# Optimization experiments

Hardware: AMD Instinct MI355X
Metric: run time of the kernel (lower is better)

Reference implementation:

```python
import jax, jax.numpy as jnp
import numpy as np

ALPHA = 0.1
K = 10


def setup_inputs() -> dict:
    key = jax.random.key(0)
    ks = jax.random.split(key, 8)
    N, E, F_IN, H, C = 100000, 1600000, 256, 128, 16
    features = jax.random.normal(ks[0], (N, F_IN), dtype=jnp.float32)
    # Kaiming-ish small init so activations stay sane
    W0 = jax.random.normal(ks[1], (F_IN, H), dtype=jnp.float32) * (1.0 / np.sqrt(F_IN))
    b0 = jnp.zeros((H,), jnp.float32)
    W1 = jax.random.normal(ks[2], (H, H), dtype=jnp.float32) * (1.0 / np.sqrt(H))
    b1 = jnp.zeros((H,), jnp.float32)
    W2 = jax.random.normal(ks[3], (H, C), dtype=jnp.float32) * (1.0 / np.sqrt(H))
    b2 = jnp.zeros((C,), jnp.float32)
    src = jax.random.randint(ks[4], (E,), 0, N, dtype=jnp.int32)
    dst = jax.random.randint(ks[5], (E,), 0, N, dtype=jnp.int32)
    return {"features": features, "W0": W0, "b0": b0, "W1": W1, "b1": b1,
            "W2": W2, "b2": b2, "src": src, "dst": dst}


def reference(features, W0, b0, W1, b1, W2, b2, src, dst):
    N = features.shape[0]
    # --- MLP feature transform (feat_drop=0 -> identity) ---
    h = jax.nn.relu(features @ W0 + b0)
    h = jax.nn.relu(h @ W1 + b1)
    h = h @ W2 + b2  # [N, C]
    # --- symmetric normalization D_out^{-1/2} A D_in^{-1/2} (DGL APPNPConv) ---
    ones = jnp.ones(src.shape[0], dtype=h.dtype)
    out_deg = jax.ops.segment_sum(ones, src, num_segments=N)
    in_deg = jax.ops.segment_sum(ones, dst, num_segments=N)
    norm_src = jnp.where(out_deg > 0, jax.lax.rsqrt(jnp.maximum(out_deg, 1.0)), 0.0)[:, None]
    norm_dst = jnp.where(in_deg > 0, jax.lax.rsqrt(jnp.maximum(in_deg, 1.0)), 0.0)[:, None]
    # --- K-step personalized PageRank propagation (edge_drop=0) ---
    h0 = h
    for _ in range(K):
        msg = (h * norm_src)[src]                         # gather [E, C]
        agg = jax.ops.segment_sum(msg, dst, num_segments=N)  # scatter-add [N, C]
        h = (1.0 - ALPHA) * (agg * norm_dst) + ALPHA * h0
    return h
```

## Files before the change

### kernel.cpp

```cpp
#include <hip/hip_runtime.h>

typedef _Float16 half8 __attribute__((ext_vector_type(8)));
typedef _Float16 half4 __attribute__((ext_vector_type(4)));
typedef float f32x4 __attribute__((ext_vector_type(4)));
typedef unsigned short u16;
typedef unsigned int u32;

constexpr int F_IN = 256;
constexpr int H    = 128;
constexpr int C    = 16;
constexpr int KITER = 10;

constexpr int RANGE = 16384;
constexpr int PCH   = 128;


__global__ __launch_bounds__(256) void hist_k(const int* __restrict__ idx,
                                              u16* __restrict__ partial,
                                              int N, int E, int R, int chunk) {
    __shared__ unsigned int cnt[RANGE / 2];
    const int p  = blockIdx.x / R;
    const int r  = blockIdx.x % R;
    const int lo = r * RANGE;
    const int hi = min(lo + RANGE, N);
    const int t  = threadIdx.x;
    for (int i = t; i < RANGE / 2; i += 256) cnt[i] = 0;
    __syncthreads();
    const int e0 = p * chunk, e1 = min(e0 + chunk, E);
    for (int e = e0 + t; e < e1; e += 256) {
        int d = idx[e];
        if (d >= lo && d < hi) {
            int dl = d - lo;
            atomicAdd(&cnt[dl >> 1], 1u << ((dl & 1) << 4));
        }
    }
    __syncthreads();
    for (int i = lo + t; i < hi; i += 256) {
        int il = i - lo;
        partial[(size_t)p * N + i] = (u16)(cnt[il >> 1] >> ((il & 1) << 4));
    }
}

__global__ __launch_bounds__(256) void hist_rank_k(const int* __restrict__ idx,
                                                   u16* __restrict__ partial,
                                                   u16* __restrict__ rank16,
                                                   int N, int E, int R, int chunk) {
    __shared__ unsigned int cnt[RANGE / 2];
    const int p  = blockIdx.x / R;
    const int r  = blockIdx.x % R;
    const int lo = r * RANGE;
    const int hi = min(lo + RANGE, N);
    const int t  = threadIdx.x;
    for (int i = t; i < RANGE / 2; i += 256) cnt[i] = 0;
    __syncthreads();
    const int e0 = p * chunk, e1 = min(e0 + chunk, E);
    for (int e = e0 + t; e < e1; e += 256) {
        int d = idx[e];
        if (d >= lo && d < hi) {
            int dl    = d - lo;
            int shift = (dl & 1) << 4;
            unsigned int old = atomicAdd(&cnt[dl >> 1], 1u << shift);
            rank16[e] = (u16)((old >> shift) & 0xffffu);
        }
    }
    __syncthreads();
    for (int i = lo + t; i < hi; i += 256) {
        int il = i - lo;
        partial[(size_t)p * N + i] = (u16)(cnt[il >> 1] >> ((il & 1) << 4));
    }
}

__global__ __launch_bounds__(256) void colsum_k(const u16* __restrict__ partial,
                                                int* __restrict__ deg, int N) {
    int i = blockIdx.x * 256 + threadIdx.x;
    if (i < N) {
        int s = 0;
#pragma unroll 8
        for (int p = 0; p < PCH; ++p) s += partial[(size_t)p * N + i];
        deg[i] = s;
    }
}

__global__ __launch_bounds__(256) void colprefix_norm_k(u16* __restrict__ partial,
                                                        const int* __restrict__ dego,
                                                        int* __restrict__ degi,
                                                        float* __restrict__ ns,
                                                        float* __restrict__ nd, int N) {
    int i = blockIdx.x * 256 + threadIdx.x;
    if (i < N) {
        int run = 0;
        for (int p = 0; p < PCH; ++p) {
            size_t q = (size_t)p * N + i;
            int v = partial[q];
            partial[q] = (u16)run;
            run += v;
        }
        degi[i] = run;
        int a = dego[i];
        ns[i] = (a > 0) ? rsqrtf((float)a) : 0.0f;
        nd[i] = (run > 0) ? rsqrtf((float)run) : 0.0f;
    }
}


__global__ __launch_bounds__(256) void scan1(const int* __restrict__ d, int* __restrict__ off,
                                             int* __restrict__ bsum, int N) {
    __shared__ int s[256];
    int t = threadIdx.x, i = blockIdx.x * 256 + t;
    int v = (i < N) ? d[i] : 0;
    s[t] = v;
    __syncthreads();
    for (int dd = 1; dd < 256; dd <<= 1) {
        int x = (t >= dd) ? s[t - dd] : 0;
        __syncthreads();
        s[t] += x;
        __syncthreads();
    }
    if (i < N) off[i] = s[t] - v;
    if (t == 255) bsum[blockIdx.x] = s[255];
}

__global__ __launch_bounds__(512) void scan2(int* __restrict__ bsum, int nb) {
    __shared__ int s[512];
    int t = threadIdx.x;
    int v = (t < nb) ? bsum[t] : 0;
    s[t] = v;
    __syncthreads();
    for (int dd = 1; dd < 512; dd <<= 1) {
        int x = (t >= dd) ? s[t - dd] : 0;
        __syncthreads();
        s[t] += x;
        __syncthreads();
    }
    if (t < nb) bsum[t] = s[t] - v;
}

__global__ __launch_bounds__(256) void scan3(int* __restrict__ off, const int* __restrict__ bsum,
                                             int N) {
    int i = blockIdx.x * 256 + threadIdx.x;
    if (i < N) off[i] += bsum[blockIdx.x];
}


__global__ __launch_bounds__(256) void scatter_pass(const int* __restrict__ src,
                                                    const int* __restrict__ dst,
                                                    const int* __restrict__ off,
                                                    const u16* __restrict__ pprefix,
                                                    const u16* __restrict__ rank16,
                                                    u32* __restrict__ epack,
                                                    int N, int E, int chunk) {
    int e = blockIdx.x * 256 + threadIdx.x;
    if (e < E) {
        int d = dst[e];
        int p = e / chunk;
        int pos = off[d] + (int)pprefix[(size_t)p * N + d] + (int)rank16[e];
        epack[pos] = (u32)src[e];
    }
}


__device__ inline void pack_one(const float* __restrict__ W, half8* __restrict__ out,
                                int tid, int NT, int Ncols) {
    int l  = tid & 63;
    int q  = tid >> 6;
    int nt = q % NT;
    int ks = q / NT;
    int col = nt * 16 + (l & 15);
    int kb  = ks * 32 + ((l >> 4) * 8);
    half8 h;
#pragma unroll
    for (int j = 0; j < 8; ++j) h[j] = (_Float16)W[(kb + j) * Ncols + col];
    out[tid] = h;
}

__global__ __launch_bounds__(256) void wpack_all(const float* __restrict__ W0,
                                                 const float* __restrict__ W1,
                                                 const float* __restrict__ W2,
                                                 half8* __restrict__ B0,
                                                 half8* __restrict__ B1,
                                                 half8* __restrict__ B2) {
    int tid = blockIdx.x * 256 + threadIdx.x;
    if (tid < 4096)      pack_one(W0, B0, tid, 8, 128);
    else if (tid < 6144) pack_one(W1, B1, tid - 4096, 8, 128);
    else if (tid < 6400) pack_one(W2, B2, tid - 6144, 1, 16);
}


__global__ __launch_bounds__(768, 3) void mlp_mega(
    const float* __restrict__ feat,
    const float4* __restrict__ Bpack,
    const float* __restrict__ b0, const float* __restrict__ b1, const float* __restrict__ b2,
    const float* __restrict__ ns,
    float* __restrict__ h0out, _Float16* __restrict__ g0out, int N)
{
    extern __shared__ char lds[];
    const half8* LB0 = (const half8*)lds;
    const half8* LB1 = (const half8*)(lds + 65536);
    const half8* LB2 = (const half8*)(lds + 98304);

    const int t  = threadIdx.x;
    const int l  = t & 63;
    const int w  = t >> 6;
    const int cl = l & 15;
    const int qk = l >> 4;
    char* swp = lds + 102400 + w * 4096;

    const int rowg = blockIdx.x * 192 + w * 16 + cl;
    const int rowc = (rowg < N) ? rowg : (N - 1);

    const float* ap = feat + (size_t)rowc * F_IN + qk * 8;
    float4 f[16];
#pragma unroll
    for (int ks = 0; ks < 8; ++ks) {
        f[2 * ks]     = *reinterpret_cast<const float4*>(ap + ks * 32);
        f[2 * ks + 1] = *reinterpret_cast<const float4*>(ap + ks * 32 + 4);
    }

    {
        float4* ldst = (float4*)lds;
        for (int i = t; i < 6400; i += 768) ldst[i] = Bpack[i];
    }
    __syncthreads();

    half8 a0[8];
#pragma unroll
    for (int ks = 0; ks < 8; ++ks) {
        half8 h;
        h[0] = (_Float16)f[2 * ks].x; h[1] = (_Float16)f[2 * ks].y;
        h[2] = (_Float16)f[2 * ks].z; h[3] = (_Float16)f[2 * ks].w;
        h[4] = (_Float16)f[2 * ks + 1].x; h[5] = (_Float16)f[2 * ks + 1].y;
        h[6] = (_Float16)f[2 * ks + 1].z; h[7] = (_Float16)f[2 * ks + 1].w;
        a0[ks] = h;
    }

    f32x4 acc0[8];
#pragma unroll
    for (int nt = 0; nt < 8; ++nt) acc0[nt] = (f32x4){0.f, 0.f, 0.f, 0.f};
#pragma unroll
    for (int ks = 0; ks < 8; ++ks)
#pragma unroll
        for (int nt = 0; nt < 8; ++nt)
            acc0[nt] = __builtin_amdgcn_mfma_f32_16x16x32_f16(a0[ks], LB0[(ks * 8 + nt) * 64 + l],
                                                              acc0[nt], 0, 0, 0);
#pragma unroll
    for (int nt = 0; nt < 8; ++nt) {
        float bb = b0[nt * 16 + cl];
#pragma unroll
        for (int r = 0; r < 4; ++r) {
            int orow = qk * 4 + r;
            int byte = orow * 256 + (((nt * 16 + cl) * 2) ^ ((orow & 7) << 4));
            *reinterpret_cast<_Float16*>(swp + byte) = (_Float16)fmaxf(acc0[nt][r] + bb, 0.0f);
        }
    }

    half8 a1[4];
#pragma unroll
    for (int ks = 0; ks < 4; ++ks) {
        int byte = cl * 256 + (((qk * 8 + ks * 32) * 2) ^ ((cl & 7) << 4));
        a1[ks] = *reinterpret_cast<const half8*>(swp + byte);
    }
    f32x4 acc1[8];
#pragma unroll
    for (int nt = 0; nt < 8; ++nt) acc1[nt] = (f32x4){0.f, 0.f, 0.f, 0.f};
#pragma unroll
    for (int ks = 0; ks < 4; ++ks)
#pragma unroll
        for (int nt = 0; nt < 8; ++nt)
            acc1[nt] = __builtin_amdgcn_mfma_f32_16x16x32_f16(a1[ks], LB1[(ks * 8 + nt) * 64 + l],
                                                              acc1[nt], 0, 0, 0);
#pragma unroll
    for (int nt = 0; nt < 8; ++nt) {
        float bb = b1[nt * 16 + cl];
#pragma unroll
        for (int r = 0; r < 4; ++r) {
            int orow = qk * 4 + r;
            int byte = orow * 256 + (((nt * 16 + cl) * 2) ^ ((orow & 7) << 4));
            *reinterpret_cast<_Float16*>(swp + byte) = (_Float16)fmaxf(acc1[nt][r] + bb, 0.0f);
        }
    }

    f32x4 acc2 = (f32x4){0.f, 0.f, 0.f, 0.f};
#pragma unroll
    for (int ks = 0; ks < 4; ++ks) {
        int byte = cl * 256 + (((qk * 8 + ks * 32) * 2) ^ ((cl & 7) << 4));
        half8 a2 = *reinterpret_cast<const half8*>(swp + byte);
        acc2 = __builtin_amdgcn_mfma_f32_16x16x32_f16(a2, LB2[ks * 64 + l], acc2, 0, 0, 0);
    }
    float bb2 = b2[cl];
#pragma unroll
    for (int r = 0; r < 4; ++r) {
        int orow = qk * 4 + r;
        int node = blockIdx.x * 192 + w * 16 + orow;
        if (node < N) {
            float hv = acc2[r] + bb2;
            h0out[(size_t)node * C + cl] = hv;
            g0out[(size_t)node * C + cl] = (_Float16)(hv * ns[node]);
        }
    }
}


__global__ __launch_bounds__(256) void gatherg(const u32* __restrict__ ep,
                                               const int* __restrict__ off,
                                               const half4* __restrict__ g,
                                               const float4* __restrict__ h0,
                                               const float* __restrict__ ns,
                                               const float* __restrict__ nd,
                                               half4* __restrict__ gnext,
                                               float4* __restrict__ hout,
                                               int N, int E, int last) {
    int gid = blockIdx.x * 256 + threadIdx.x;
    int node = gid >> 2;
    if (node >= N) return;
    int c = gid & 3;
    int o0 = off[node];
    int o1 = (node + 1 < N) ? off[node + 1] : E;
    float k  = 0.9f * nd[node];
    float sc = ns[node];
    float4 hv = h0[gid];
    float4 aA = {0.f, 0.f, 0.f, 0.f};
    float4 aB = {0.f, 0.f, 0.f, 0.f};
    float4 aC = {0.f, 0.f, 0.f, 0.f};
    float4 aD = {0.f, 0.f, 0.f, 0.f};
    int o = o0;
    for (; o + 8 <= o1; o += 8) {
        int s0 = (int)ep[o];     int s1 = (int)ep[o + 1];
        int s2 = (int)ep[o + 2]; int s3 = (int)ep[o + 3];
        int s4 = (int)ep[o + 4]; int s5 = (int)ep[o + 5];
        int s6 = (int)ep[o + 6]; int s7 = (int)ep[o + 7];
        half4 x0 = g[s0 * 4 + c]; half4 x1 = g[s1 * 4 + c];
        half4 x2 = g[s2 * 4 + c]; half4 x3 = g[s3 * 4 + c];
        half4 x4 = g[s4 * 4 + c]; half4 x5 = g[s5 * 4 + c];
        half4 x6 = g[s6 * 4 + c]; half4 x7 = g[s7 * 4 + c];
        aA.x += (float)x0[0]; aA.y += (float)x0[1]; aA.z += (float)x0[2]; aA.w += (float)x0[3];
        aB.x += (float)x1[0]; aB.y += (float)x1[1]; aB.z += (float)x1[2]; aB.w += (float)x1[3];
        aC.x += (float)x2[0]; aC.y += (float)x2[1]; aC.z += (float)x2[2]; aC.w += (float)x2[3];
        aD.x += (float)x3[0]; aD.y += (float)x3[1]; aD.z += (float)x3[2]; aD.w += (float)x3[3];
        aA.x += (float)x4[0]; aA.y += (float)x4[1]; aA.z += (float)x4[2]; aA.w += (float)x4[3];
        aB.x += (float)x5[0]; aB.y += (float)x5[1]; aB.z += (float)x5[2]; aB.w += (float)x5[3];
        aC.x += (float)x6[0]; aC.y += (float)x6[1]; aC.z += (float)x6[2]; aC.w += (float)x6[3];
        aD.x += (float)x7[0]; aD.y += (float)x7[1]; aD.z += (float)x7[2]; aD.w += (float)x7[3];
    }
    for (; o + 2 <= o1; o += 2) {
        int s0 = (int)ep[o];
        int s1 = (int)ep[o + 1];
        half4 x0 = g[s0 * 4 + c];
        half4 x1 = g[s1 * 4 + c];
        aA.x += (float)x0[0]; aA.y += (float)x0[1]; aA.z += (float)x0[2]; aA.w += (float)x0[3];
        aB.x += (float)x1[0]; aB.y += (float)x1[1]; aB.z += (float)x1[2]; aB.w += (float)x1[3];
    }
    if (o < o1) {
        int s0 = (int)ep[o];
        half4 x0 = g[s0 * 4 + c];
        aA.x += (float)x0[0]; aA.y += (float)x0[1]; aA.z += (float)x0[2]; aA.w += (float)x0[3];
    }
    aA.x += aB.x + aC.x + aD.x;
    aA.y += aB.y + aC.y + aD.y;
    aA.z += aB.z + aC.z + aD.z;
    aA.w += aB.w + aC.w + aD.w;
    float4 res;
    res.x = fmaf(k, aA.x, 0.1f * hv.x);
    res.y = fmaf(k, aA.y, 0.1f * hv.y);
    res.z = fmaf(k, aA.z, 0.1f * hv.z);
    res.w = fmaf(k, aA.w, 0.1f * hv.w);
    if (last) {
        hout[gid] = res;
    } else {
        half4 gv;
        gv[0] = (_Float16)(res.x * sc);
        gv[1] = (_Float16)(res.y * sc);
        gv[2] = (_Float16)(res.z * sc);
        gv[3] = (_Float16)(res.w * sc);
        gnext[gid] = gv;
    }
}


extern "C" void kernel_launch(void* const* d_in, const int* in_sizes, int n_in,
                              void* d_out, int out_size, void* d_ws, size_t ws_size,
                              hipStream_t stream) {
    const float* feat = (const float*)d_in[0];
    const float* W0   = (const float*)d_in[1];
    const float* b0   = (const float*)d_in[2];
    const float* W1   = (const float*)d_in[3];
    const float* b1   = (const float*)d_in[4];
    const float* W2   = (const float*)d_in[5];
    const float* b2   = (const float*)d_in[6];
    const int*   src  = (const int*)d_in[7];
    const int*   dst  = (const int*)d_in[8];

    const int N = in_sizes[0] / F_IN;
    const int E = in_sizes[7];
    const int NB = (N + 255) / 256;
    const int R  = (N + RANGE - 1) / RANGE;
    const int chunk = (E + PCH - 1) / PCH;

    char* base = (char*)d_ws;
    u16* part = (u16*)base;
    float*    h0 = (float*)base;
    _Float16* g0 = (_Float16*)(base + (size_t)N * C * 4);
    _Float16* ga = (_Float16*)(base + (size_t)N * C * 6);
    _Float16* gb = (_Float16*)(base + (size_t)N * C * 8);
    char* ws = base + (size_t)PCH * N * 2;
    int*   dego = (int*)ws;   ws += (size_t)N * 4;
    int*   degi = (int*)ws;   ws += (size_t)N * 4;
    float* ns   = (float*)ws; ws += (size_t)N * 4;
    float* nd   = (float*)ws; ws += (size_t)N * 4;
    int*   off  = (int*)ws;   ws += (size_t)N * 4;
    int*   bsum = (int*)ws;   ws += 512 * 4;
    u16*   rank16 = (u16*)ws; ws += (size_t)E * 2;
    u32*   epack  = (u32*)ws; ws += (size_t)E * 4;
    half8* B0 = (half8*)ws;   ws += 4096 * 16;
    half8* B1 = (half8*)ws;   ws += 2048 * 16;
    half8* B2 = (half8*)ws;   ws += 256 * 16;

    hist_k<<<PCH * R, 256, 0, stream>>>(src, part, N, E, R, chunk);
    colsum_k<<<NB, 256, 0, stream>>>(part, dego, N);
    hist_rank_k<<<PCH * R, 256, 0, stream>>>(dst, part, rank16, N, E, R, chunk);
    colprefix_norm_k<<<NB, 256, 0, stream>>>(part, dego, degi, ns, nd, N);

    scan1<<<NB, 256, 0, stream>>>(degi, off, bsum, N);
    scan2<<<1, 512, 0, stream>>>(bsum, NB);
    scan3<<<NB, 256, 0, stream>>>(off, bsum, N);
    scatter_pass<<<(E + 255) / 256, 256, 0, stream>>>(src, dst, off, part, rank16, epack, N, E, chunk);

    wpack_all<<<25, 256, 0, stream>>>(W0, W1, W2, B0, B1, B2);
    mlp_mega<<<(N + 191) / 192, 768, 151552, stream>>>(feat, (const float4*)B0, b0, b1, b2,
                                                       ns, h0, g0, N);

    const _Float16* curg = g0;
    for (int it = 0; it < KITER; ++it) {
        int last = (it == KITER - 1);
        _Float16* nxtg = (it & 1) ? gb : ga;
        gatherg<<<(N * 4 + 255) / 256, 256, 0, stream>>>(epack, off, (const half4*)curg,
                                                         (const float4*)h0, ns, nd,
                                                         (half4*)nxtg, (float4*)d_out, N, E, last);
        curg = nxtg;
    }
}
```

Before: 345.2 us.

## Coalesce MLP feature loads via LDS staging and fuse column prefix with scan

The MLP kernel now loads the 64-row feature tile with fully coalesced float4 reads, converts it to fp16 into a swizzled LDS buffer, and then reads the MFMA A fragments from there. The packed weights are read straight from global memory or cache instead of being copied into 150KB of LDS per block, and blocks shrink to 256 threads. Separately, the column-prefix/normalisation kernel is fused with the first level of the offset scan, which removes the degi array and one launch. The risk is that weight fragments now come from global/L2 inside the MFMA loops instead of from LDS.

```diff
diff --git a/kernel.cpp b/kernel.cpp
--- a/kernel.cpp
+++ b/kernel.cpp
@@ -81,34 +81,27 @@
     }
 }
 
-__global__ __launch_bounds__(256) void colprefix_norm_k(u16* __restrict__ partial,
-                                                        const int* __restrict__ dego,
-                                                        int* __restrict__ degi,
-                                                        float* __restrict__ ns,
-                                                        float* __restrict__ nd, int N) {
-    int i = blockIdx.x * 256 + threadIdx.x;
+__global__ __launch_bounds__(256) void colprefix_norm_scan_k(u16* __restrict__ partial,
+                                                             const int* __restrict__ dego,
+                                                             float* __restrict__ ns,
+                                                             float* __restrict__ nd,
+                                                             int* __restrict__ off,
+                                                             int* __restrict__ bsum, int N) {
+    __shared__ int s[256];
+    int t = threadIdx.x, i = blockIdx.x * 256 + t;
+    int run = 0;
     if (i < N) {
-        int run = 0;
         for (int p = 0; p < PCH; ++p) {
             size_t q = (size_t)p * N + i;
             int v = partial[q];
             partial[q] = (u16)run;
             run += v;
         }
-        degi[i] = run;
         int a = dego[i];
         ns[i] = (a > 0) ? rsqrtf((float)a) : 0.0f;
         nd[i] = (run > 0) ? rsqrtf((float)run) : 0.0f;
     }
-}
-
-
-__global__ __launch_bounds__(256) void scan1(const int* __restrict__ d, int* __restrict__ off,
-                                             int* __restrict__ bsum, int N) {
-    __shared__ int s[256];
-    int t = threadIdx.x, i = blockIdx.x * 256 + t;
-    int v = (i < N) ? d[i] : 0;
-    s[t] = v;
+    s[t] = run;
     __syncthreads();
     for (int dd = 1; dd < 256; dd <<= 1) {
         int x = (t >= dd) ? s[t - dd] : 0;
@@ -116,7 +109,7 @@
         s[t] += x;
         __syncthreads();
     }
-    if (i < N) off[i] = s[t] - v;
+    if (i < N) off[i] = s[t] - run;
     if (t == 255) bsum[blockIdx.x] = s[255];
 }
 
@@ -186,52 +179,50 @@
 }
 
 
-__global__ __launch_bounds__(768, 3) void mlp_mega(
+__global__ __launch_bounds__(256, 3) void mlp_coal(
     const float* __restrict__ feat,
-    const float4* __restrict__ Bpack,
-    const float* __restrict__ b0, const float* __restrict__ b1, const float* __restrict__ b2,
+    const half8* __restrict__ B0, const float* __restrict__ b0,
+    const half8* __restrict__ B1, const float* __restrict__ b1,
+    const half8* __restrict__ B2, const float* __restrict__ b2,
     const float* __restrict__ ns,
     float* __restrict__ h0out, _Float16* __restrict__ g0out, int N)
 {
-    extern __shared__ char lds[];
-    const half8* LB0 = (const half8*)lds;
-    const half8* LB1 = (const half8*)(lds + 65536);
-    const half8* LB2 = (const half8*)(lds + 98304);
-
+    __shared__ __align__(16) char sF[64 * 512];
     const int t  = threadIdx.x;
     const int l  = t & 63;
     const int w  = t >> 6;
     const int cl = l & 15;
     const int qk = l >> 4;
-    char* swp = lds + 102400 + w * 4096;
-
-    const int rowg = blockIdx.x * 192 + w * 16 + cl;
-    const int rowc = (rowg < N) ? rowg : (N - 1);
-
-    const float* ap = feat + (size_t)rowc * F_IN + qk * 8;
-    float4 f[16];
+
+    {
+        const float4* g4 = reinterpret_cast<const float4*>(feat);
+        const size_t qbase = (size_t)blockIdx.x * 4096;
+        const size_t maxq  = (size_t)N * 64 - 1;
+#pragma unroll
+        for (int i = 0; i < 16; ++i) {
+            size_t q = qbase + i * 256 + t;
+            if (q > maxq) q = maxq;
+            float4 a = g4[q];
+            int lq   = i * 256 + t;
+            int row  = lq >> 6;
+            int colb = (lq & 63) * 8;
+            int byte = row * 512 + (colb ^ ((row & 7) << 4));
+            half4 h = {(_Float16)a.x, (_Float16)a.y, (_Float16)a.z, (_Float16)a.w};
+            *reinterpret_cast<half4*>(sF + byte) = h;
+        }
+    }
+    __syncthreads();
+
+    const int arow = w * 16 + cl;
+    half8 a0[8];
 #pragma unroll
     for (int ks = 0; ks < 8; ++ks) {
-        f[2 * ks]     = *reinterpret_cast<const float4*>(ap + ks * 32);
-        f[2 * ks + 1] = *reinterpret_cast<const float4*>(ap + ks * 32 + 4);
-    }
-
-    {
-        float4* ldst = (float4*)lds;
-        for (int i = t; i < 6400; i += 768) ldst[i] = Bpack[i];
-    }
-    __syncthreads();
-
-    half8 a0[8];
-#pragma unroll
-    for (int ks = 0; ks < 8; ++ks) {
-        half8 h;
-        h[0] = (_Float16)f[2 * ks].x; h[1] = (_Float16)f[2 * ks].y;
-        h[2] = (_Float16)f[2 * ks].z; h[3] = (_Float16)f[2 * ks].w;
-        h[4] = (_Float16)f[2 * ks + 1].x; h[5] = (_Float16)f[2 * ks + 1].y;
-        h[6] = (_Float16)f[2 * ks + 1].z; h[7] = (_Float16)f[2 * ks + 1].w;
-        a0[ks] = h;
-    }
+        int byte = arow * 512 + (((ks * 64) + qk * 16) ^ ((arow & 7) << 4));
+        a0[ks] = *reinterpret_cast<const half8*>(sF + byte);
+    }
+    __syncthreads();
+
+    char* swp = sF + w * 4096;
 
     f32x4 acc0[8];
 #pragma unroll
@@ -240,7 +231,7 @@
     for (int ks = 0; ks < 8; ++ks)
 #pragma unroll
         for (int nt = 0; nt < 8; ++nt)
-            acc0[nt] = __builtin_amdgcn_mfma_f32_16x16x32_f16(a0[ks], LB0[(ks * 8 + nt) * 64 + l],
+            acc0[nt] = __builtin_amdgcn_mfma_f32_16x16x32_f16(a0[ks], B0[(ks * 8 + nt) * 64 + l],
                                                               acc0[nt], 0, 0, 0);
 #pragma unroll
     for (int nt = 0; nt < 8; ++nt) {
@@ -266,7 +257,7 @@
     for (int ks = 0; ks < 4; ++ks)
 #pragma unroll
         for (int nt = 0; nt < 8; ++nt)
-            acc1[nt] = __builtin_amdgcn_mfma_f32_16x16x32_f16(a1[ks], LB1[(ks * 8 + nt) * 64 + l],
+            acc1[nt] = __builtin_amdgcn_mfma_f32_16x16x32_f16(a1[ks], B1[(ks * 8 + nt) * 64 + l],
                                                               acc1[nt], 0, 0, 0);
 #pragma unroll
     for (int nt = 0; nt < 8; ++nt) {
@@ -284,13 +275,13 @@
     for (int ks = 0; ks < 4; ++ks) {
         int byte = cl * 256 + (((qk * 8 + ks * 32) * 2) ^ ((cl & 7) << 4));
         half8 a2 = *reinterpret_cast<const half8*>(swp + byte);
-        acc2 = __builtin_amdgcn_mfma_f32_16x16x32_f16(a2, LB2[ks * 64 + l], acc2, 0, 0, 0);
+        acc2 = __builtin_amdgcn_mfma_f32_16x16x32_f16(a2, B2[ks * 64 + l], acc2, 0, 0, 0);
     }
     float bb2 = b2[cl];
 #pragma unroll
     for (int r = 0; r < 4; ++r) {
         int orow = qk * 4 + r;
-        int node = blockIdx.x * 192 + w * 16 + orow;
+        int node = blockIdx.x * 64 + w * 16 + orow;
         if (node < N) {
             float hv = acc2[r] + bb2;
             h0out[(size_t)node * C + cl] = hv;
@@ -403,7 +394,6 @@
     _Float16* gb = (_Float16*)(base + (size_t)N * C * 8);
     char* ws = base + (size_t)PCH * N * 2;
     int*   dego = (int*)ws;   ws += (size_t)N * 4;
-    int*   degi = (int*)ws;   ws += (size_t)N * 4;
     float* ns   = (float*)ws; ws += (size_t)N * 4;
     float* nd   = (float*)ws; ws += (size_t)N * 4;
     int*   off  = (int*)ws;   ws += (size_t)N * 4;
@@ -417,16 +407,14 @@
     hist_k<<<PCH * R, 256, 0, stream>>>(src, part, N, E, R, chunk);
     colsum_k<<<NB, 256, 0, stream>>>(part, dego, N);
     hist_rank_k<<<PCH * R, 256, 0, stream>>>(dst, part, rank16, N, E, R, chunk);
-    colprefix_norm_k<<<NB, 256, 0, stream>>>(part, dego, degi, ns, nd, N);
-
-    scan1<<<NB, 256, 0, stream>>>(degi, off, bsum, N);
+    colprefix_norm_scan_k<<<NB, 256, 0, stream>>>(part, dego, ns, nd, off, bsum, N);
+
     scan2<<<1, 512, 0, stream>>>(bsum, NB);
     scan3<<<NB, 256, 0, stream>>>(off, bsum, N);
     scatter_pass<<<(E + 255) / 256, 256, 0, stream>>>(src, dst, off, part, rank16, epack, N, E, chunk);
 
     wpack_all<<<25, 256, 0, stream>>>(W0, W1, W2, B0, B1, B2);
-    mlp_mega<<<(N + 191) / 192, 768, 151552, stream>>>(feat, (const float4*)B0, b0, b1, b2,
-                                                       ns, h0, g0, N);
+    mlp_coal<<<(N + 63) / 64, 256, 0, stream>>>(feat, B0, b0, B1, b1, B2, b2, ns, h0, g0, N);
 
     const _Float16* curg = g0;
     for (int it = 0; it < KITER; ++it) {
```

Measured after the change: 355.2 us. 1.03x slower.
